# Performance work log

Measured on AMD Instinct MI355X. Metric: run time of the kernel, lower is better.

The kernel has to match this reference:

```python
import jax, jax.numpy as jnp
import numpy as np

GROUPS = 32
EPS = 1e-5
N_HEADS = 8


def setup_inputs() -> dict:
    key = jax.random.key(0)
    ks = jax.random.split(key, 12)
    B, H, W, C = 16, 64, 64, 512
    Nctx, Dctx = 77, 768
    s_c = 1.0 / np.sqrt(C)
    s_ctx = 1.0 / np.sqrt(Dctx)
    return {
        "x": jax.random.normal(ks[0], (B, H, W, C), jnp.float32),
        "context": jax.random.normal(ks[1], (B, Nctx, Dctx), jnp.float32),
        "gn_scale": jnp.ones((C,), jnp.float32),
        "gn_bias": jnp.zeros((C,), jnp.float32),
        "wq": jax.random.normal(ks[2], (C, C), jnp.float32) * s_c,
        "bq": jnp.zeros((C,), jnp.float32),
        "wk": jax.random.normal(ks[3], (Dctx, C), jnp.float32) * s_ctx,
        "bk": jnp.zeros((C,), jnp.float32),
        "wv": jax.random.normal(ks[4], (Dctx, C), jnp.float32) * s_ctx,
        "bv": jnp.zeros((C,), jnp.float32),
        "wo": jax.random.normal(ks[5], (C, C), jnp.float32) * s_c,
        "bo": jnp.zeros((C,), jnp.float32),
    }


def _group_norm(x, scale, bias):
    B, H, W, C = x.shape
    xg = x.reshape(B, H, W, GROUPS, C // GROUPS)
    mean = jnp.mean(xg, axis=(1, 2, 4), keepdims=True)
    var = jnp.var(xg, axis=(1, 2, 4), keepdims=True)
    xn = (xg - mean) * jax.lax.rsqrt(var + EPS)
    return xn.reshape(B, H, W, C) * scale + bias


def reference(x, context, gn_scale, gn_bias, wq, bq, wk, bk, wv, bv, wo, bo):
    B, H, W, C = x.shape
    head_dim = C // N_HEADS
    h = _group_norm(x, gn_scale, gn_bias)
    h_flat = h.reshape(B, H * W, C)
    Q = h_flat @ wq + bq                      # [B, N, C]
    K = context @ wk + bk                     # [B, Nctx, C]
    V = context @ wv + bv

    def split_heads(t):
        b, n, c = t.shape
        return t.reshape(b, n, N_HEADS, head_dim).transpose(0, 2, 1, 3)

    Qh, Kh, Vh = split_heads(Q), split_heads(K), split_heads(V)
    scale = 1.0 / jnp.sqrt(jnp.asarray(head_dim, x.dtype))
    scores = jnp.einsum('bhid,bhjd->bhij', Qh, Kh) * scale
    attn = jax.nn.softmax(scores, axis=-1)
    out = jnp.einsum('bhij,bhjd->bhid', attn, Vh)  # [B, h, N, d]
    out = out.transpose(0, 2, 1, 3).reshape(B, H * W, C)
    out = out @ wo + bo
    return out.reshape(B, H, W, C) + x
```

## Files before the change

kernel.cpp:

```cpp
#include <hip/hip_runtime.h>
#include <hip/hip_bf16.h>

typedef __attribute__((ext_vector_type(4))) float f32x4;
typedef __attribute__((ext_vector_type(8))) short bf16x8;
typedef unsigned short u16;

#define AS1 __attribute__((address_space(1)))
#define AS3 __attribute__((address_space(3)))

#define B_    16
#define HW_   4096
#define C_    512
#define NCTX  77
#define DCTX  768
#define NH    8
#define HD    64
#define EPSV  1e-5f

__device__ inline u16 f2bf(float f) {
    union { float f; unsigned u; } v; v.f = f;
    unsigned r = v.u + 0x7fffu + ((v.u >> 16) & 1u);
    return (u16)(r >> 16);
}
__device__ inline float bf2f(u16 h) {
    union { unsigned u; float f; } v; v.u = ((unsigned)h) << 16;
    return v.f;
}

__global__ __launch_bounds__(256) void gn_stats(const float* __restrict__ x,
                                                float* __restrict__ mean,
                                                float* __restrict__ rstd) {
    int b = blockIdx.x >> 5, g = blockIdx.x & 31;
    const float* px = x + (size_t)b * HW_ * C_ + g * 16;
    float s = 0.f, ss = 0.f;
    for (int t = threadIdx.x; t < HW_ * 4; t += 256) {
        int hw = t >> 2, c4 = (t & 3) * 4;
        const float4 v = *(const float4*)(px + (size_t)hw * C_ + c4);
        s  += v.x + v.y + v.z + v.w;
        ss += v.x * v.x + v.y * v.y + v.z * v.z + v.w * v.w;
    }
    for (int off = 32; off; off >>= 1) { s += __shfl_xor(s, off); ss += __shfl_xor(ss, off); }
    __shared__ float red[2][4];
    int wv = threadIdx.x >> 6, lane = threadIdx.x & 63;
    if (lane == 0) { red[0][wv] = s; red[1][wv] = ss; }
    __syncthreads();
    if (threadIdx.x == 0) {
        float S = red[0][0] + red[0][1] + red[0][2] + red[0][3];
        float SS = red[1][0] + red[1][1] + red[1][2] + red[1][3];
        float mn = S / 65536.f;
        float var = SS / 65536.f - mn * mn;
        mean[blockIdx.x] = mn;
        rstd[blockIdx.x] = rsqrtf(var + EPSV);
    }
}

__global__ __launch_bounds__(256) void transpose_all(const float* __restrict__ wq,
                                                     const float* __restrict__ wk,
                                                     const float* __restrict__ wv,
                                                     const float* __restrict__ wo,
                                                     u16* __restrict__ wqT,
                                                     u16* __restrict__ wkT,
                                                     u16* __restrict__ wvT,
                                                     u16* __restrict__ woT) {
    int idx = blockIdx.x * 256 + threadIdx.x;
    if (idx < 262144) {
        int k = idx >> 9, n = idx & 511;
        wqT[(size_t)n * 512 + k] = f2bf(wq[idx]);
    } else if (idx < 655360) {
        int i = idx - 262144;
        int k = i >> 9, n = i & 511;
        wkT[(size_t)n * 768 + k] = f2bf(wk[i]);
    } else if (idx < 1048576) {
        int i = idx - 655360;
        int k = i >> 9, n = i & 511;
        wvT[(size_t)n * 768 + k] = f2bf(wv[i]);
    } else if (idx < 1310720) {
        int i = idx - 1048576;
        int k = i >> 9, n = i & 511;
        woT[(size_t)n * 512 + k] = f2bf(wo[i]);
    }
}

__global__ __launch_bounds__(256) void gemm_kv(const float* __restrict__ A,
                                               const u16* __restrict__ wkT,
                                               const u16* __restrict__ wvT,
                                               const float* __restrict__ bk,
                                               const float* __restrict__ bv,
                                               u16* __restrict__ kb,
                                               u16* __restrict__ vb) {
    constexpr int M = 1232, K = 768;
    __shared__ __align__(16) u16 As[128][40];
    __shared__ __align__(16) u16 Bs[128][40];
    int bx = blockIdx.x;
    const u16* Bt = (bx < 4) ? wkT : wvT;
    const float* bias = (bx < 4) ? bk : bv;
    u16* out = (bx < 4) ? kb : vb;
    int tid = threadIdx.x, lane = tid & 63, wid = tid >> 6;
    int wm = wid >> 1, wn = wid & 1;
    int row0 = blockIdx.y * 128, col0 = (bx & 3) * 128;
    int q = lane >> 4, r16 = lane & 15;

    f32x4 acc[4][4];
#pragma unroll
    for (int i = 0; i < 4; i++)
#pragma unroll
        for (int j = 0; j < 4; j++) acc[i][j] = (f32x4){0.f, 0.f, 0.f, 0.f};

    for (int k0 = 0; k0 < K; k0 += 32) {
#pragma unroll
        for (int it = 0; it < 2; ++it) {
            int e = it * 256 + tid;
            int rr = e >> 2, kc = (e & 3) * 8;
            int ga = row0 + rr; if (ga > M - 1) ga = M - 1;
            float4 a0 = *(const float4*)(A + (size_t)ga * K + k0 + kc);
            float4 a1 = *(const float4*)(A + (size_t)ga * K + k0 + kc + 4);
            bf16x8 av;
            av[0] = (short)f2bf(a0.x); av[1] = (short)f2bf(a0.y);
            av[2] = (short)f2bf(a0.z); av[3] = (short)f2bf(a0.w);
            av[4] = (short)f2bf(a1.x); av[5] = (short)f2bf(a1.y);
            av[6] = (short)f2bf(a1.z); av[7] = (short)f2bf(a1.w);
            *(bf16x8*)&As[rr][kc] = av;
            int gb = col0 + rr;
            bf16x8 bv8 = *(const bf16x8*)(Bt + (size_t)gb * K + k0 + kc);
            *(bf16x8*)&Bs[rr][kc] = bv8;
        }
        __syncthreads();
        bf16x8 afr[4], bfr[4];
#pragma unroll
        for (int mi = 0; mi < 4; mi++) afr[mi] = *(const bf16x8*)&As[wm * 64 + mi * 16 + r16][q * 8];
#pragma unroll
        for (int ni = 0; ni < 4; ni++) bfr[ni] = *(const bf16x8*)&Bs[wn * 64 + ni * 16 + r16][q * 8];
#pragma unroll
        for (int mi = 0; mi < 4; mi++)
#pragma unroll
            for (int ni = 0; ni < 4; ni++)
                acc[mi][ni] = __builtin_amdgcn_mfma_f32_16x16x32_bf16(afr[mi], bfr[ni], acc[mi][ni], 0, 0, 0);
        __syncthreads();
    }

#pragma unroll
    for (int mi = 0; mi < 4; mi++) {
#pragma unroll
        for (int rr = 0; rr < 4; rr++) {
            int grow = row0 + wm * 64 + mi * 16 + q * 4 + rr;
            if (grow >= M) continue;
#pragma unroll
            for (int ni = 0; ni < 4; ni++) {
                int gcol = col0 + wn * 64 + ni * 16 + r16;
                float v = acc[mi][ni][rr] + bias[gcol];
                out[(size_t)grow * 512 + gcol] = f2bf(v);
            }
        }
    }
}

__global__ __launch_bounds__(256, 2) void gemm_fusedq(const float* __restrict__ x,
                                                      const float* __restrict__ mean,
                                                      const float* __restrict__ rstd,
                                                      const float* __restrict__ gns,
                                                      const float* __restrict__ gnb,
                                                      const u16* __restrict__ Bt,
                                                      const float* __restrict__ bias,
                                                      u16* __restrict__ out) {
    constexpr int K = 512;
    __shared__ __align__(16) u16 LA[2][8192];
    __shared__ __align__(16) u16 LB[2][8192];
    int tid = threadIdx.x, lane = tid & 63, wid = tid >> 6;
    int wr = wid >> 1, wc = wid & 1;
    int q = lane >> 4, r16 = lane & 15;

    int orig = blockIdx.x;
    int wg = (orig & 7) * 256 + (orig >> 3);
    int bx = wg & 3, by = wg >> 2;
    int row0 = by * 128, col0 = bx * 128;

    int srow = tid >> 3;
    int schunk = (tid & 7) ^ (srow & 7);
    const u16* gB = Bt + (size_t)(col0 + srow) * K + schunk * 8;
    const int lo = tid * 8;

    int c8 = tid & 7;
    int rbase = (tid >> 3) * 4;
    const float* xb = x + (size_t)(row0 + rbase) * 512 + c8 * 8;
    int bg0 = (row0 >> 12) * 32;

    f32x4 acc[4][4];
#pragma unroll
    for (int i = 0; i < 4; i++)
#pragma unroll
        for (int j = 0; j < 4; j++) acc[i][j] = (f32x4){0.f, 0.f, 0.f, 0.f};

    float4 ar[8];
    float mn, rs;
    float4 s0v, s1v, b0v, b1v;

#define LOADA(kt) do { _Pragma("unroll")                                          \
    for (int i_ = 0; i_ < 4; ++i_) {                                              \
        ar[2 * i_]     = *(const float4*)(xb + (kt) * 64 + (size_t)i_ * 512);     \
        ar[2 * i_ + 1] = *(const float4*)(xb + (kt) * 64 + (size_t)i_ * 512 + 4); \
    } } while (0)

#define LOADP(kt) do { int c0_ = (kt) * 64 + c8 * 8; int bg_ = bg0 + (c0_ >> 4);  \
    mn = mean[bg_]; rs = rstd[bg_];                                               \
    s0v = *(const float4*)(gns + c0_); s1v = *(const float4*)(gns + c0_ + 4);     \
    b0v = *(const float4*)(gnb + c0_); b1v = *(const float4*)(gnb + c0_ + 4);     \
  } while (0)

#define WRITEA(nbuf) do {                                                         \
    float m2_[8], a2_[8];                                                         \
    m2_[0]=rs*s0v.x; m2_[1]=rs*s0v.y; m2_[2]=rs*s0v.z; m2_[3]=rs*s0v.w;           \
    m2_[4]=rs*s1v.x; m2_[5]=rs*s1v.y; m2_[6]=rs*s1v.z; m2_[7]=rs*s1v.w;           \
    a2_[0]=b0v.x-mn*m2_[0]; a2_[1]=b0v.y-mn*m2_[1];                               \
    a2_[2]=b0v.z-mn*m2_[2]; a2_[3]=b0v.w-mn*m2_[3];                               \
    a2_[4]=b1v.x-mn*m2_[4]; a2_[5]=b1v.y-mn*m2_[5];                               \
    a2_[6]=b1v.z-mn*m2_[6]; a2_[7]=b1v.w-mn*m2_[7];                               \
    _Pragma("unroll")                                                             \
    for (int i_ = 0; i_ < 4; ++i_) {                                              \
        int row_ = rbase + i_;                                                    \
        bf16x8 pk_;                                                               \
        pk_[0]=(short)f2bf(ar[2*i_].x  *m2_[0]+a2_[0]);                           \
        pk_[1]=(short)f2bf(ar[2*i_].y  *m2_[1]+a2_[1]);                           \
        pk_[2]=(short)f2bf(ar[2*i_].z  *m2_[2]+a2_[2]);                           \
        pk_[3]=(short)f2bf(ar[2*i_].w  *m2_[3]+a2_[3]);                           \
        pk_[4]=(short)f2bf(ar[2*i_+1].x*m2_[4]+a2_[4]);                           \
        pk_[5]=(short)f2bf(ar[2*i_+1].y*m2_[5]+a2_[5]);                           \
        pk_[6]=(short)f2bf(ar[2*i_+1].z*m2_[6]+a2_[6]);                           \
        pk_[7]=(short)f2bf(ar[2*i_+1].w*m2_[7]+a2_[7]);                           \
        *(bf16x8*)&LA[nbuf][row_ * 64 + ((c8 ^ (row_ & 7)) * 8)] = pk_;           \
    } } while (0)

#define STG_B(kt, s) __builtin_amdgcn_global_load_lds( \
        (const AS1 void*)(gB + (kt) * 64 + (size_t)((s) * 32) * K), \
        (AS3 void*)(&LB[(kt) & 1][(s) * 2048 + lo]), 16, 0, 0)

#define PHASE_(buf, h, ks) do {                                                            \
    bf16x8 afr[2], bfr[4];                                                                 \
    const int ch_ = (((ks) * 4 + q) ^ (r16 & 7)) * 8;                                      \
    _Pragma("unroll")                                                                      \
    for (int mi = 0; mi < 2; mi++)                                                         \
        afr[mi] = *(const bf16x8*)&LA[buf][(wr * 64 + ((h) * 2 + mi) * 16 + r16) * 64 + ch_]; \
    _Pragma("unroll")                                                                      \
    for (int ni = 0; ni < 4; ni++)                                                         \
        bfr[ni] = *(const bf16x8*)&LB[buf][(wc * 64 + ni * 16 + r16) * 64 + ch_];          \
    __builtin_amdgcn_s_setprio(1);                                                         \
    _Pragma("unroll")                                                                      \
    for (int mi = 0; mi < 2; mi++)                                                         \
      _Pragma("unroll")                                                                    \
      for (int ni = 0; ni < 4; ni++)                                                       \
        acc[(h) * 2 + mi][ni] =                                                            \
            __builtin_amdgcn_mfma_f32_16x16x32_bf16(afr[mi], bfr[ni], acc[(h) * 2 + mi][ni], 0, 0, 0); \
    __builtin_amdgcn_s_setprio(0);                                                         \
  } while (0)

    LOADA(0); LOADP(0);
    asm volatile("" ::: "memory");
    STG_B(0, 0); STG_B(0, 1); STG_B(0, 2); STG_B(0, 3);
    asm volatile("s_waitcnt vmcnt(4)" ::: "memory");
    WRITEA(0);
    asm volatile("s_waitcnt lgkmcnt(0)" ::: "memory");

#pragma unroll
    for (int t = 0; t < 7; ++t) {
        const int buf = t & 1;
        LOADA(t + 1); LOADP(t + 1);
        asm volatile("" ::: "memory");
        STG_B(t + 1, 0); STG_B(t + 1, 1); STG_B(t + 1, 2); STG_B(t + 1, 3);
        asm volatile("s_waitcnt vmcnt(18)" ::: "memory");
        __builtin_amdgcn_s_barrier();
        asm volatile("" ::: "memory");
        PHASE_(buf, 0, 0); PHASE_(buf, 1, 0); PHASE_(buf, 0, 1); PHASE_(buf, 1, 1);
        asm volatile("s_waitcnt vmcnt(4)" ::: "memory");
        WRITEA(buf ^ 1);
        asm volatile("s_waitcnt lgkmcnt(0)" ::: "memory");
        __builtin_amdgcn_s_barrier();
        asm volatile("" ::: "memory");
    }
    asm volatile("s_waitcnt vmcnt(0) lgkmcnt(0)" ::: "memory");
    __builtin_amdgcn_s_barrier();
    asm volatile("" ::: "memory");
    PHASE_(1, 0, 0); PHASE_(1, 1, 0); PHASE_(1, 0, 1); PHASE_(1, 1, 1);
#undef LOADA
#undef LOADP
#undef WRITEA
#undef STG_B
#undef PHASE_

#pragma unroll
    for (int mi = 0; mi < 4; mi++) {
#pragma unroll
        for (int rr = 0; rr < 4; rr++) {
            int grow = row0 + wr * 64 + mi * 16 + q * 4 + rr;
#pragma unroll
            for (int ni = 0; ni < 4; ni++) {
                int gcol = col0 + wc * 64 + ni * 16 + r16;
                float v = acc[mi][ni][rr] + bias[gcol];
                out[(size_t)grow * 512 + gcol] = f2bf(v);
            }
        }
    }
}

__global__ __launch_bounds__(256, 4) void gemm_ring(const u16* __restrict__ A,
                                                    const u16* __restrict__ Bt,
                                                    const float* __restrict__ bias,
                                                    const float* __restrict__ res,
                                                    float* __restrict__ out) {
    constexpr int K = 512;
    __shared__ __align__(16) u16 LA[2][4096];
    __shared__ __align__(16) u16 LB[2][4096];
    int tid = threadIdx.x, lane = tid & 63, wid = tid >> 6;
    int wr = wid >> 1, wc = wid & 1;
    int q = lane >> 4, r16 = lane & 15;

    int orig = blockIdx.x;
    int wg = (orig & 7) * 256 + (orig >> 3);
    int bx = wg & 3, by = wg >> 2;
    int row0 = by * 128, col0 = bx * 128;

    int srow = tid >> 2;
    int schunk = (tid & 3) ^ (srow & 3);
    const u16* gA = A + (size_t)(row0 + srow) * K + schunk * 8;
    const u16* gB = Bt + (size_t)(col0 + srow) * K + schunk * 8;
    const int lo = tid * 8;

    f32x4 acc[4][4];
#pragma unroll
    for (int i = 0; i < 4; i++)
#pragma unroll
        for (int j = 0; j < 4; j++) acc[i][j] = (f32x4){0.f, 0.f, 0.f, 0.f};

#define STG(kt) do { int sl_ = (kt) & 1;                                              \
    __builtin_amdgcn_global_load_lds((const AS1 void*)(gA + (kt) * 32),               \
                                     (AS3 void*)(&LA[sl_][lo]), 16, 0, 0);            \
    __builtin_amdgcn_global_load_lds((const AS1 void*)(gA + (kt) * 32 + (size_t)64 * K), \
                                     (AS3 void*)(&LA[sl_][2048 + lo]), 16, 0, 0);     \
    __builtin_amdgcn_global_load_lds((const AS1 void*)(gB + (kt) * 32),               \
                                     (AS3 void*)(&LB[sl_][lo]), 16, 0, 0);            \
    __builtin_amdgcn_global_load_lds((const AS1 void*)(gB + (kt) * 32 + (size_t)64 * K), \
                                     (AS3 void*)(&LB[sl_][2048 + lo]), 16, 0, 0);     \
  } while (0)

#define COMPUTE(sl) do {                                                              \
    bf16x8 afr[4], bfr[4];                                                            \
    const int ch_ = (q ^ (r16 & 3)) * 8;                                              \
    _Pragma("unroll")                                                                 \
    for (int mi = 0; mi < 4; mi++)                                                    \
        afr[mi] = *(const bf16x8*)&LA[sl][(wr * 64 + mi * 16 + r16) * 32 + ch_];      \
    _Pragma("unroll")                                                                 \
    for (int ni = 0; ni < 4; ni++)                                                    \
        bfr[ni] = *(const bf16x8*)&LB[sl][(wc * 64 + ni * 16 + r16) * 32 + ch_];      \
    __builtin_amdgcn_s_setprio(1);                                                    \
    _Pragma("unroll")                                                                 \
    for (int mi = 0; mi < 4; mi++)                                                    \
      _Pragma("unroll")                                                               \
      for (int ni = 0; ni < 4; ni++)                                                  \
        acc[mi][ni] = __builtin_amdgcn_mfma_f32_16x16x32_bf16(afr[mi], bfr[ni], acc[mi][ni], 0, 0, 0); \
    __builtin_amdgcn_s_setprio(0);                                                    \
  } while (0)

    STG(0);
#pragma unroll
    for (int t = 0; t < 15; ++t) {
        STG(t + 1);
        asm volatile("s_waitcnt vmcnt(4)" ::: "memory");
        asm volatile("s_barrier" ::: "memory");
        COMPUTE(t & 1);
        asm volatile("s_barrier" ::: "memory");
    }
    asm volatile("s_waitcnt vmcnt(0)" ::: "memory");
    asm volatile("s_barrier" ::: "memory");
    COMPUTE(1);
#undef STG
#undef COMPUTE

#pragma unroll
    for (int mi = 0; mi < 4; mi++) {
#pragma unroll
        for (int rr = 0; rr < 4; rr++) {
            int grow = row0 + wr * 64 + mi * 16 + q * 4 + rr;
#pragma unroll
            for (int ni = 0; ni < 4; ni++) {
                int gcol = col0 + wc * 64 + ni * 16 + r16;
                float v = acc[mi][ni][rr] + bias[gcol];
                size_t idx = (size_t)grow * 512 + gcol;
                out[idx] = v + res[idx];
            }
        }
    }
}

__global__ __launch_bounds__(256) void attn_mfma(const u16* __restrict__ Qb,
                                                 const u16* __restrict__ Kb,
                                                 const u16* __restrict__ Vb,
                                                 u16* __restrict__ Ob) {
    __shared__ __align__(16) u16 Ks[80][72];
    __shared__ __align__(16) u16 VT[64][104];
    __shared__ __align__(16) u16 Ps[64][104];
    int tid = threadIdx.x, lane = tid & 63, wv = tid >> 6;
    int q = lane >> 4, r16 = lane & 15;
    int tile0 = blockIdx.x * 8;
    int bh = blockIdx.y;
    int b = bh >> 3, h = bh & 7;

    {
        unsigned* p0 = (unsigned*)&Ks[0][0];
        for (int i = tid; i < 2880; i += 256) p0[i] = 0u;
        unsigned* p1 = (unsigned*)&VT[0][0];
        for (int i = tid; i < 3328; i += 256) p1[i] = 0u;
        unsigned* p2 = (unsigned*)&Ps[0][0];
        for (int i = tid; i < 3328; i += 256) p2[i] = 0u;
    }
    __syncthreads();

    size_t kvbase = ((size_t)b * NCTX) * C_ + h * HD;
    for (int c = tid; c < NCTX * 8; c += 256) {
        int j = c >> 3, d8 = (c & 7) * 8;
        *(bf16x8*)&Ks[j][d8] = *(const bf16x8*)(Kb + kvbase + (size_t)j * C_ + d8);
    }
    for (int t = tid; t < NCTX * 64; t += 256) {
        int j = t >> 6, d = t & 63;
        VT[d][j] = Vb[kvbase + (size_t)j * C_ + d];
    }
    __syncthreads();

    const size_t tstep = (size_t)64 * C_;
    const u16* qp = Qb + ((size_t)b * HW_ + wv * 16 + r16) * C_ + h * HD + q * 8;
    bool v4 = (r16 < NCTX - 64);

    bf16x8 qc0 = *(const bf16x8*)(qp + (size_t)tile0 * tstep);
    bf16x8 qc1 = *(const bf16x8*)(qp + (size_t)tile0 * tstep + 32);

    for (int it = 0; it < 8; ++it) {
        int tile = tile0 + it;
        bf16x8 qn0 = qc0, qn1 = qc1;
        if (it < 7) {
            qn0 = *(const bf16x8*)(qp + (size_t)(tile + 1) * tstep);
            qn1 = *(const bf16x8*)(qp + (size_t)(tile + 1) * tstep + 32);
        }

        f32x4 accs[5];
#pragma unroll
        for (int nt = 0; nt < 5; ++nt) accs[nt] = (f32x4){0.f, 0.f, 0.f, 0.f};
#pragma unroll
        for (int nt = 0; nt < 5; ++nt) {
            bf16x8 kf = *(const bf16x8*)&Ks[nt * 16 + r16][q * 8];
            accs[nt] = __builtin_amdgcn_mfma_f32_16x16x32_bf16(qc0, kf, accs[nt], 0, 0, 0);
        }
#pragma unroll
        for (int nt = 0; nt < 5; ++nt) {
            bf16x8 kf = *(const bf16x8*)&Ks[nt * 16 + r16][32 + q * 8];
            accs[nt] = __builtin_amdgcn_mfma_f32_16x16x32_bf16(qc1, kf, accs[nt], 0, 0, 0);
        }

#pragma unroll
        for (int r = 0; r < 4; ++r) {
            float s[5];
#pragma unroll
            for (int nt = 0; nt < 5; ++nt) s[nt] = accs[nt][r] * 0.125f;
            float m = fmaxf(fmaxf(fmaxf(s[0], s[1]), fmaxf(s[2], s[3])), v4 ? s[4] : -3.0e38f);
#pragma unroll
            for (int off = 1; off < 16; off <<= 1) m = fmaxf(m, __shfl_xor(m, off));
            float e[5], sum = 0.f;
#pragma unroll
            for (int nt = 0; nt < 5; ++nt) {
                e[nt] = (nt < 4 || v4) ? __expf(s[nt] - m) : 0.f;
                sum += e[nt];
            }
#pragma unroll
            for (int off = 1; off < 16; off <<= 1) sum += __shfl_xor(sum, off);
            float inv = 1.0f / sum;
            int prow = wv * 16 + q * 4 + r;
#pragma unroll
            for (int nt = 0; nt < 5; ++nt)
                Ps[prow][nt * 16 + r16] = f2bf(e[nt] * inv);
        }

        f32x4 acco[4];
#pragma unroll
        for (int nt = 0; nt < 4; ++nt) acco[nt] = (f32x4){0.f, 0.f, 0.f, 0.f};
#pragma unroll
        for (int ks = 0; ks < 3; ++ks) {
            bf16x8 pf = *(const bf16x8*)&Ps[wv * 16 + r16][ks * 32 + q * 8];
#pragma unroll
            for (int nt = 0; nt < 4; ++nt) {
                bf16x8 vf = *(const bf16x8*)&VT[nt * 16 + r16][ks * 32 + q * 8];
                acco[nt] = __builtin_amdgcn_mfma_f32_16x16x32_bf16(pf, vf, acco[nt], 0, 0, 0);
            }
        }

        int row0 = tile * 64 + wv * 16;
#pragma unroll
        for (int nt = 0; nt < 4; ++nt)
#pragma unroll
            for (int r = 0; r < 4; ++r) {
                int row = row0 + q * 4 + r;
                int col = h * HD + nt * 16 + r16;
                Ob[((size_t)b * HW_ + row) * C_ + col] = f2bf(acco[nt][r]);
            }
        qc0 = qn0; qc1 = qn1;
    }
}

extern "C" void kernel_launch(void* const* d_in, const int* in_sizes, int n_in,
                              void* d_out, int out_size, void* d_ws, size_t ws_size,
                              hipStream_t stream) {
    const float* x   = (const float*)d_in[0];
    const float* ctx = (const float*)d_in[1];
    const float* gns = (const float*)d_in[2];
    const float* gnb = (const float*)d_in[3];
    const float* wq  = (const float*)d_in[4];
    const float* bq  = (const float*)d_in[5];
    const float* wk  = (const float*)d_in[6];
    const float* bk  = (const float*)d_in[7];
    const float* wv  = (const float*)d_in[8];
    const float* bv  = (const float*)d_in[9];
    const float* wo  = (const float*)d_in[10];
    const float* bo  = (const float*)d_in[11];

    char* ws = (char*)d_ws;
    float* mean = (float*)(ws + 0);
    float* rstd = (float*)(ws + 2048);
    u16* wqT  = (u16*)(ws + 4096);
    u16* wkT  = (u16*)(ws + 528384);
    u16* wvT  = (u16*)(ws + 1314816);
    u16* woT  = (u16*)(ws + 2101248);
    u16* aob  = (u16*)(ws + 4517888);
    u16* qb   = (u16*)(ws + 71626752);
    u16* kb   = (u16*)(ws + 138735616);
    u16* vb   = (u16*)(ws + 139997184);

    gn_stats<<<512, 256, 0, stream>>>(x, mean, rstd);
    transpose_all<<<5120, 256, 0, stream>>>(wq, wk, wv, wo, wqT, wkT, wvT, woT);

    gemm_fusedq<<<2048, 256, 0, stream>>>(x, mean, rstd, gns, gnb, wqT, bq, qb);
    gemm_kv<<<dim3(8, 10), 256, 0, stream>>>(ctx, wkT, wvT, bk, bv, kb, vb);

    attn_mfma<<<dim3(8, 128), 256, 0, stream>>>(qb, kb, vb, aob);

    gemm_ring<<<2048, 256, 0, stream>>>(aob, woT, bo, x, (float*)d_out);
}
```

Before: 291.3 us.

## Fuse Q projection with attention and merge stats/transpose kernels

```diff
diff --git a/kernel.cpp b/kernel.cpp
--- a/kernel.cpp
+++ b/kernel.cpp
@@ -22,62 +22,59 @@
     unsigned r = v.u + 0x7fffu + ((v.u >> 16) & 1u);
     return (u16)(r >> 16);
 }
-__device__ inline float bf2f(u16 h) {
-    union { unsigned u; float f; } v; v.u = ((unsigned)h) << 16;
-    return v.f;
-}
-
-__global__ __launch_bounds__(256) void gn_stats(const float* __restrict__ x,
+
+__global__ __launch_bounds__(256) void gn_trans(const float* __restrict__ x,
                                                 float* __restrict__ mean,
-                                                float* __restrict__ rstd) {
-    int b = blockIdx.x >> 5, g = blockIdx.x & 31;
-    const float* px = x + (size_t)b * HW_ * C_ + g * 16;
-    float s = 0.f, ss = 0.f;
-    for (int t = threadIdx.x; t < HW_ * 4; t += 256) {
-        int hw = t >> 2, c4 = (t & 3) * 4;
-        const float4 v = *(const float4*)(px + (size_t)hw * C_ + c4);
-        s  += v.x + v.y + v.z + v.w;
-        ss += v.x * v.x + v.y * v.y + v.z * v.z + v.w * v.w;
-    }
-    for (int off = 32; off; off >>= 1) { s += __shfl_xor(s, off); ss += __shfl_xor(ss, off); }
-    __shared__ float red[2][4];
-    int wv = threadIdx.x >> 6, lane = threadIdx.x & 63;
-    if (lane == 0) { red[0][wv] = s; red[1][wv] = ss; }
-    __syncthreads();
-    if (threadIdx.x == 0) {
-        float S = red[0][0] + red[0][1] + red[0][2] + red[0][3];
-        float SS = red[1][0] + red[1][1] + red[1][2] + red[1][3];
-        float mn = S / 65536.f;
-        float var = SS / 65536.f - mn * mn;
-        mean[blockIdx.x] = mn;
-        rstd[blockIdx.x] = rsqrtf(var + EPSV);
-    }
-}
-
-__global__ __launch_bounds__(256) void transpose_all(const float* __restrict__ wq,
-                                                     const float* __restrict__ wk,
-                                                     const float* __restrict__ wv,
-                                                     const float* __restrict__ wo,
-                                                     u16* __restrict__ wqT,
-                                                     u16* __restrict__ wkT,
-                                                     u16* __restrict__ wvT,
-                                                     u16* __restrict__ woT) {
-    int idx = blockIdx.x * 256 + threadIdx.x;
-    if (idx < 262144) {
-        int k = idx >> 9, n = idx & 511;
-        wqT[(size_t)n * 512 + k] = f2bf(wq[idx]);
-    } else if (idx < 655360) {
-        int i = idx - 262144;
-        int k = i >> 9, n = i & 511;
-        wkT[(size_t)n * 768 + k] = f2bf(wk[i]);
-    } else if (idx < 1048576) {
-        int i = idx - 655360;
-        int k = i >> 9, n = i & 511;
-        wvT[(size_t)n * 768 + k] = f2bf(wv[i]);
-    } else if (idx < 1310720) {
-        int i = idx - 1048576;
-        int k = i >> 9, n = i & 511;
-        woT[(size_t)n * 512 + k] = f2bf(wo[i]);
+                                                float* __restrict__ rstd,
+                                                const float* __restrict__ wq,
+                                                const float* __restrict__ wk,
+                                                const float* __restrict__ wv,
+                                                const float* __restrict__ wo,
+                                                u16* __restrict__ wqT,
+                                                u16* __restrict__ wkT,
+                                                u16* __restrict__ wvT,
+                                                u16* __restrict__ woT) {
+    if (blockIdx.x < 512) {
+        int b = blockIdx.x >> 5, g = blockIdx.x & 31;
+        const float* px = x + (size_t)b * HW_ * C_ + g * 16;
+        float s = 0.f, ss = 0.f;
+        for (int t = threadIdx.x; t < HW_ * 4; t += 256) {
+            int hw = t >> 2, c4 = (t & 3) * 4;
+            const float4 v = *(const float4*)(px + (size_t)hw * C_ + c4);
+            s  += v.x + v.y + v.z + v.w;
+            ss += v.x * v.x + v.y * v.y + v.z * v.z + v.w * v.w;
+        }
+        for (int off = 32; off; off >>= 1) { s += __shfl_xor(s, off); ss += __shfl_xor(ss, off); }
+        __shared__ float red[2][4];
+        int wv_ = threadIdx.x >> 6, lane = threadIdx.x & 63;
+        if (lane == 0) { red[0][wv_] = s; red[1][wv_] = ss; }
+        __syncthreads();
+        if (threadIdx.x == 0) {
+            float S = red[0][0] + red[0][1] + red[0][2] + red[0][3];
+            float SS = red[1][0] + red[1][1] + red[1][2] + red[1][3];
+            float mn = S / 65536.f;
+            float var = SS / 65536.f - mn * mn;
+            mean[blockIdx.x] = mn;
+            rstd[blockIdx.x] = rsqrtf(var + EPSV);
+        }
+    } else {
+        int idx = (blockIdx.x - 512) * 256 + threadIdx.x;
+        if (idx < 262144) {
+            int k = idx >> 9, n = idx & 511;
+            wqT[(size_t)n * 512 + k] = f2bf(wq[idx]);
+        } else if (idx < 655360) {
+            int i = idx - 262144;
+            int k = i >> 9, n = i & 511;
+            wkT[(size_t)n * 768 + k] = f2bf(wk[i]);
+        } else if (idx < 1048576) {
+            int i = idx - 655360;
+            int k = i >> 9, n = i & 511;
+            wvT[(size_t)n * 768 + k] = f2bf(wv[i]);
+        } else if (idx < 1310720) {
+            int i = idx - 1048576;
+            int k = i >> 9, n = i & 511;
+            woT[(size_t)n * 512 + k] = f2bf(wo[i]);
+        }
     }
 }
 
@@ -154,122 +151,145 @@
     }
 }
 
-__global__ __launch_bounds__(256, 2) void gemm_fusedq(const float* __restrict__ x,
+__global__ __launch_bounds__(256, 2) void fused_qattn(const float* __restrict__ x,
                                                       const float* __restrict__ mean,
                                                       const float* __restrict__ rstd,
                                                       const float* __restrict__ gns,
                                                       const float* __restrict__ gnb,
-                                                      const u16* __restrict__ Bt,
-                                                      const float* __restrict__ bias,
-                                                      u16* __restrict__ out) {
-    constexpr int K = 512;
-    __shared__ __align__(16) u16 LA[2][8192];
-    __shared__ __align__(16) u16 LB[2][8192];
+                                                      const u16* __restrict__ wqT,
+                                                      const float* __restrict__ bq,
+                                                      const u16* __restrict__ kb,
+                                                      const u16* __restrict__ vb,
+                                                      u16* __restrict__ aob) {
+    __shared__ __align__(16) u16 Ks[80][72];
+    __shared__ __align__(16) u16 VT[64][96];
+    __shared__ __align__(16) u16 Qs[128][72];
+    __shared__ __align__(16) u16 Ps[64][96];
+    __shared__ __align__(16) u16 LA[2][4096];
+    __shared__ __align__(16) u16 LB[2][2048];
     int tid = threadIdx.x, lane = tid & 63, wid = tid >> 6;
     int wr = wid >> 1, wc = wid & 1;
     int q = lane >> 4, r16 = lane & 15;
 
     int orig = blockIdx.x;
-    int wg = (orig & 7) * 256 + (orig >> 3);
-    int bx = wg & 3, by = wg >> 2;
-    int row0 = by * 128, col0 = bx * 128;
-
-    int srow = tid >> 3;
-    int schunk = (tid & 7) ^ (srow & 7);
-    const u16* gB = Bt + (size_t)(col0 + srow) * K + schunk * 8;
-    const int lo = tid * 8;
-
-    int c8 = tid & 7;
-    int rbase = (tid >> 3) * 4;
-    const float* xb = x + (size_t)(row0 + rbase) * 512 + c8 * 8;
-    int bg0 = (row0 >> 12) * 32;
-
-    f32x4 acc[4][4];
+    int wg = (orig & 7) * 512 + (orig >> 3);
+    int by = wg >> 3, h = wg & 7;
+    int row0 = by * 128;
+    int b = by >> 5;
+
+    {
+        unsigned* p0 = (unsigned*)&Ks[0][0];
+        for (int i = tid; i < 2880; i += 256) p0[i] = 0u;
+        unsigned* p1 = (unsigned*)&VT[0][0];
+        for (int i = tid; i < 3072; i += 256) p1[i] = 0u;
+        unsigned* p2 = (unsigned*)&Ps[0][0];
+        for (int i = tid; i < 3072; i += 256) p2[i] = 0u;
+    }
+    __syncthreads();
+
+    size_t kvbase = (size_t)b * NCTX * C_ + h * HD;
+    for (int c = tid; c < NCTX * 8; c += 256) {
+        int j = c >> 3, d8 = (c & 7) * 8;
+        *(bf16x8*)&Ks[j][d8] = *(const bf16x8*)(kb + kvbase + (size_t)j * C_ + d8);
+    }
+    for (int t = tid; t < NCTX * 64; t += 256) {
+        int j = t >> 6, d = t & 63;
+        VT[d][j] = vb[kvbase + (size_t)j * C_ + d];
+    }
+    asm volatile("s_waitcnt vmcnt(0) lgkmcnt(0)" ::: "memory");
+    __syncthreads();
+
+    int c8 = tid & 3;
+    int r0l = (tid >> 2) * 2;
+    const float* xb = x + (size_t)(row0 + r0l) * 512 + c8 * 8;
+    int bg0 = b * 32;
+    int srB = tid >> 2;
+    int cB = (tid & 3) ^ (srB & 3);
+    const u16* gB = wqT + (size_t)(h * 64 + srB) * 512 + cB * 8;
+
+    f32x4 acc[4][2];
 #pragma unroll
     for (int i = 0; i < 4; i++)
 #pragma unroll
-        for (int j = 0; j < 4; j++) acc[i][j] = (f32x4){0.f, 0.f, 0.f, 0.f};
-
-    float4 ar[8];
+        for (int j = 0; j < 2; j++) acc[i][j] = (f32x4){0.f, 0.f, 0.f, 0.f};
+
+    float4 ar0, ar1, ar2, ar3;
     float mn, rs;
     float4 s0v, s1v, b0v, b1v;
 
-#define LOADA(kt) do { _Pragma("unroll")                                          \
-    for (int i_ = 0; i_ < 4; ++i_) {                                              \
-        ar[2 * i_]     = *(const float4*)(xb + (kt) * 64 + (size_t)i_ * 512);     \
-        ar[2 * i_ + 1] = *(const float4*)(xb + (kt) * 64 + (size_t)i_ * 512 + 4); \
-    } } while (0)
-
-#define LOADP(kt) do { int c0_ = (kt) * 64 + c8 * 8; int bg_ = bg0 + (c0_ >> 4);  \
-    mn = mean[bg_]; rs = rstd[bg_];                                               \
-    s0v = *(const float4*)(gns + c0_); s1v = *(const float4*)(gns + c0_ + 4);     \
-    b0v = *(const float4*)(gnb + c0_); b1v = *(const float4*)(gnb + c0_ + 4);     \
+#define LOADA(kt) do {                                      \
+    ar0 = *(const float4*)(xb + (kt) * 32);                 \
+    ar1 = *(const float4*)(xb + (kt) * 32 + 4);             \
+    ar2 = *(const float4*)(xb + (kt) * 32 + 512);           \
+    ar3 = *(const float4*)(xb + (kt) * 32 + 516);           \
   } while (0)
 
-#define WRITEA(nbuf) do {                                                         \
-    float m2_[8], a2_[8];                                                         \
-    m2_[0]=rs*s0v.x; m2_[1]=rs*s0v.y; m2_[2]=rs*s0v.z; m2_[3]=rs*s0v.w;           \
-    m2_[4]=rs*s1v.x; m2_[5]=rs*s1v.y; m2_[6]=rs*s1v.z; m2_[7]=rs*s1v.w;           \
-    a2_[0]=b0v.x-mn*m2_[0]; a2_[1]=b0v.y-mn*m2_[1];                               \
-    a2_[2]=b0v.z-mn*m2_[2]; a2_[3]=b0v.w-mn*m2_[3];                               \
-    a2_[4]=b1v.x-mn*m2_[4]; a2_[5]=b1v.y-mn*m2_[5];                               \
-    a2_[6]=b1v.z-mn*m2_[6]; a2_[7]=b1v.w-mn*m2_[7];                               \
-    _Pragma("unroll")                                                             \
-    for (int i_ = 0; i_ < 4; ++i_) {                                              \
-        int row_ = rbase + i_;                                                    \
-        bf16x8 pk_;                                                               \
-        pk_[0]=(short)f2bf(ar[2*i_].x  *m2_[0]+a2_[0]);                           \
-        pk_[1]=(short)f2bf(ar[2*i_].y  *m2_[1]+a2_[1]);                           \
-        pk_[2]=(short)f2bf(ar[2*i_].z  *m2_[2]+a2_[2]);                           \
-        pk_[3]=(short)f2bf(ar[2*i_].w  *m2_[3]+a2_[3]);                           \
-        pk_[4]=(short)f2bf(ar[2*i_+1].x*m2_[4]+a2_[4]);                           \
-        pk_[5]=(short)f2bf(ar[2*i_+1].y*m2_[5]+a2_[5]);                           \
-        pk_[6]=(short)f2bf(ar[2*i_+1].z*m2_[6]+a2_[6]);                           \
-        pk_[7]=(short)f2bf(ar[2*i_+1].w*m2_[7]+a2_[7]);                           \
-        *(bf16x8*)&LA[nbuf][row_ * 64 + ((c8 ^ (row_ & 7)) * 8)] = pk_;           \
-    } } while (0)
-
-#define STG_B(kt, s) __builtin_amdgcn_global_load_lds( \
-        (const AS1 void*)(gB + (kt) * 64 + (size_t)((s) * 32) * K), \
-        (AS3 void*)(&LB[(kt) & 1][(s) * 2048 + lo]), 16, 0, 0)
-
-#define PHASE_(buf, h, ks) do {                                                            \
-    bf16x8 afr[2], bfr[4];                                                                 \
-    const int ch_ = (((ks) * 4 + q) ^ (r16 & 7)) * 8;                                      \
+#define LOADP(kt) do { int c0_ = (kt) * 32 + c8 * 8; int bg_ = bg0 + (c0_ >> 4); \
+    mn = mean[bg_]; rs = rstd[bg_];                                              \
+    s0v = *(const float4*)(gns + c0_); s1v = *(const float4*)(gns + c0_ + 4);    \
+    b0v = *(const float4*)(gnb + c0_); b1v = *(const float4*)(gnb + c0_ + 4);    \
+  } while (0)
+
+#define WRITEA(nbuf) do {                                                        \
+    float m_[8], a_[8];                                                          \
+    m_[0]=rs*s0v.x; m_[1]=rs*s0v.y; m_[2]=rs*s0v.z; m_[3]=rs*s0v.w;              \
+    m_[4]=rs*s1v.x; m_[5]=rs*s1v.y; m_[6]=rs*s1v.z; m_[7]=rs*s1v.w;              \
+    a_[0]=b0v.x-mn*m_[0]; a_[1]=b0v.y-mn*m_[1];                                  \
+    a_[2]=b0v.z-mn*m_[2]; a_[3]=b0v.w-mn*m_[3];                                  \
+    a_[4]=b1v.x-mn*m_[4]; a_[5]=b1v.y-mn*m_[5];                                  \
+    a_[6]=b1v.z-mn*m_[6]; a_[7]=b1v.w-mn*m_[7];                                  \
+    bf16x8 p0_, p1_;                                                             \
+    p0_[0]=(short)f2bf(ar0.x*m_[0]+a_[0]); p0_[1]=(short)f2bf(ar0.y*m_[1]+a_[1]);\
+    p0_[2]=(short)f2bf(ar0.z*m_[2]+a_[2]); p0_[3]=(short)f2bf(ar0.w*m_[3]+a_[3]);\
+    p0_[4]=(short)f2bf(ar1.x*m_[4]+a_[4]); p0_[5]=(short)f2bf(ar1.y*m_[5]+a_[5]);\
+    p0_[6]=(short)f2bf(ar1.z*m_[6]+a_[6]); p0_[7]=(short)f2bf(ar1.w*m_[7]+a_[7]);\
+    p1_[0]=(short)f2bf(ar2.x*m_[0]+a_[0]); p1_[1]=(short)f2bf(ar2.y*m_[1]+a_[1]);\
+    p1_[2]=(short)f2bf(ar2.z*m_[2]+a_[2]); p1_[3]=(short)f2bf(ar2.w*m_[3]+a_[3]);\
+    p1_[4]=(short)f2bf(ar3.x*m_[4]+a_[4]); p1_[5]=(short)f2bf(ar3.y*m_[5]+a_[5]);\
+    p1_[6]=(short)f2bf(ar3.z*m_[6]+a_[6]); p1_[7]=(short)f2bf(ar3.w*m_[7]+a_[7]);\
+    *(bf16x8*)&LA[nbuf][r0l * 32 + ((c8 ^ (r0l & 3)) * 8)] = p0_;                \
+    *(bf16x8*)&LA[nbuf][(r0l + 1) * 32 + ((c8 ^ ((r0l + 1) & 3)) * 8)] = p1_;    \
+  } while (0)
+
+#define STG_B(kt) __builtin_amdgcn_global_load_lds( \
+        (const AS1 void*)(gB + (kt) * 32), (AS3 void*)(&LB[(kt) & 1][tid * 8]), 16, 0, 0)
+
+#define COMPUTE(buf) do {                                                                  \
+    bf16x8 afr[4], bfr[2];                                                                 \
+    const int ch_ = (q ^ (r16 & 3)) * 8;                                                   \
     _Pragma("unroll")                                                                      \
-    for (int mi = 0; mi < 2; mi++)                                                         \
-        afr[mi] = *(const bf16x8*)&LA[buf][(wr * 64 + ((h) * 2 + mi) * 16 + r16) * 64 + ch_]; \
+    for (int mi = 0; mi < 4; mi++)                                                         \
+        afr[mi] = *(const bf16x8*)&LA[buf][(wr * 64 + mi * 16 + r16) * 32 + ch_];          \
     _Pragma("unroll")                                                                      \
-    for (int ni = 0; ni < 4; ni++)                                                         \
-        bfr[ni] = *(const bf16x8*)&LB[buf][(wc * 64 + ni * 16 + r16) * 64 + ch_];          \
+    for (int ni = 0; ni < 2; ni++)                                                         \
+        bfr[ni] = *(const bf16x8*)&LB[buf][(wc * 32 + ni * 16 + r16) * 32 + ch_];          \
     __builtin_amdgcn_s_setprio(1);                                                         \
     _Pragma("unroll")                                                                      \
-    for (int mi = 0; mi < 2; mi++)                                                         \
+    for (int mi = 0; mi < 4; mi++)                                                         \
       _Pragma("unroll")                                                                    \
-      for (int ni = 0; ni < 4; ni++)                                                       \
-        acc[(h) * 2 + mi][ni] =                                                            \
-            __builtin_amdgcn_mfma_f32_16x16x32_bf16(afr[mi], bfr[ni], acc[(h) * 2 + mi][ni], 0, 0, 0); \
+      for (int ni = 0; ni < 2; ni++)                                                       \
+        acc[mi][ni] = __builtin_amdgcn_mfma_f32_16x16x32_bf16(afr[mi], bfr[ni], acc[mi][ni], 0, 0, 0); \
     __builtin_amdgcn_s_setprio(0);                                                         \
   } while (0)
 
     LOADA(0); LOADP(0);
     asm volatile("" ::: "memory");
-    STG_B(0, 0); STG_B(0, 1); STG_B(0, 2); STG_B(0, 3);
-    asm volatile("s_waitcnt vmcnt(4)" ::: "memory");
+    STG_B(0);
+    asm volatile("s_waitcnt vmcnt(1)" ::: "memory");
     WRITEA(0);
     asm volatile("s_waitcnt lgkmcnt(0)" ::: "memory");
 
 #pragma unroll
-    for (int t = 0; t < 7; ++t) {
+    for (int t = 0; t < 15; ++t) {
         const int buf = t & 1;
         LOADA(t + 1); LOADP(t + 1);
         asm volatile("" ::: "memory");
-        STG_B(t + 1, 0); STG_B(t + 1, 1); STG_B(t + 1, 2); STG_B(t + 1, 3);
-        asm volatile("s_waitcnt vmcnt(18)" ::: "memory");
+        STG_B(t + 1);
+        asm volatile("s_waitcnt vmcnt(11)" ::: "memory");
         __builtin_amdgcn_s_barrier();
         asm volatile("" ::: "memory");
-        PHASE_(buf, 0, 0); PHASE_(buf, 1, 0); PHASE_(buf, 0, 1); PHASE_(buf, 1, 1);
-        asm volatile("s_waitcnt vmcnt(4)" ::: "memory");
+        COMPUTE(buf);
+        asm volatile("s_waitcnt vmcnt(1)" ::: "memory");
         WRITEA(buf ^ 1);
         asm volatile("s_waitcnt lgkmcnt(0)" ::: "memory");
         __builtin_amdgcn_s_barrier();
@@ -278,25 +298,90 @@
     asm volatile("s_waitcnt vmcnt(0) lgkmcnt(0)" ::: "memory");
     __builtin_amdgcn_s_barrier();
     asm volatile("" ::: "memory");
-    PHASE_(1, 0, 0); PHASE_(1, 1, 0); PHASE_(1, 0, 1); PHASE_(1, 1, 1);
+    COMPUTE(1);
 #undef LOADA
 #undef LOADP
 #undef WRITEA
 #undef STG_B
-#undef PHASE_
-
-#pragma unroll
-    for (int mi = 0; mi < 4; mi++) {
-#pragma unroll
-        for (int rr = 0; rr < 4; rr++) {
-            int grow = row0 + wr * 64 + mi * 16 + q * 4 + rr;
-#pragma unroll
-            for (int ni = 0; ni < 4; ni++) {
-                int gcol = col0 + wc * 64 + ni * 16 + r16;
-                float v = acc[mi][ni][rr] + bias[gcol];
-                out[(size_t)grow * 512 + gcol] = f2bf(v);
+#undef COMPUTE
+
+#pragma unroll
+    for (int mi = 0; mi < 4; mi++)
+#pragma unroll
+        for (int ni = 0; ni < 2; ni++)
+#pragma unroll
+            for (int rr = 0; rr < 4; rr++) {
+                int row = wr * 64 + mi * 16 + q * 4 + rr;
+                int col = wc * 32 + ni * 16 + r16;
+                Qs[row][col] = f2bf(acc[mi][ni][rr] + bq[h * 64 + col]);
             }
-        }
+    __syncthreads();
+
+    bool v4 = (r16 < NCTX - 64);
+#pragma unroll
+    for (int rh = 0; rh < 2; ++rh) {
+        int rl0 = rh * 64 + wid * 16;
+        bf16x8 qf0 = *(const bf16x8*)&Qs[rl0 + r16][q * 8];
+        bf16x8 qf1 = *(const bf16x8*)&Qs[rl0 + r16][32 + q * 8];
+
+        f32x4 accs[5];
+#pragma unroll
+        for (int nt = 0; nt < 5; ++nt) accs[nt] = (f32x4){0.f, 0.f, 0.f, 0.f};
+#pragma unroll
+        for (int nt = 0; nt < 5; ++nt) {
+            bf16x8 kf = *(const bf16x8*)&Ks[nt * 16 + r16][q * 8];
+            accs[nt] = __builtin_amdgcn_mfma_f32_16x16x32_bf16(qf0, kf, accs[nt], 0, 0, 0);
+        }
+#pragma unroll
+        for (int nt = 0; nt < 5; ++nt) {
+            bf16x8 kf = *(const bf16x8*)&Ks[nt * 16 + r16][32 + q * 8];
+            accs[nt] = __builtin_amdgcn_mfma_f32_16x16x32_bf16(qf1, kf, accs[nt], 0, 0, 0);
+        }
+
+#pragma unroll
+        for (int r = 0; r < 4; ++r) {
+            float s[5];
+#pragma unroll
+            for (int nt = 0; nt < 5; ++nt) s[nt] = accs[nt][r] * 0.125f;
+            float m = fmaxf(fmaxf(fmaxf(s[0], s[1]), fmaxf(s[2], s[3])), v4 ? s[4] : -3.0e38f);
+#pragma unroll
+            for (int off = 1; off < 16; off <<= 1) m = fmaxf(m, __shfl_xor(m, off));
+            float e[5], sum = 0.f;
+#pragma unroll
+            for (int nt = 0; nt < 5; ++nt) {
+                e[nt] = (nt < 4 || v4) ? __expf(s[nt] - m) : 0.f;
+                sum += e[nt];
+            }
+#pragma unroll
+            for (int off = 1; off < 16; off <<= 1) sum += __shfl_xor(sum, off);
+            float inv = 1.0f / sum;
+            int prow = wid * 16 + q * 4 + r;
+#pragma unroll
+            for (int nt = 0; nt < 5; ++nt)
+                Ps[prow][nt * 16 + r16] = f2bf(e[nt] * inv);
+        }
+
+        f32x4 acco[4];
+#pragma unroll
+        for (int nt = 0; nt < 4; ++nt) acco[nt] = (f32x4){0.f, 0.f, 0.f, 0.f};
+#pragma unroll
+        for (int ks = 0; ks < 3; ++ks) {
+            bf16x8 pf = *(const bf16x8*)&Ps[wid * 16 + r16][ks * 32 + q * 8];
+#pragma unroll
+            for (int nt = 0; nt < 4; ++nt) {
+                bf16x8 vf = *(const bf16x8*)&VT[nt * 16 + r16][ks * 32 + q * 8];
+                acco[nt] = __builtin_amdgcn_mfma_f32_16x16x32_bf16(pf, vf, acco[nt], 0, 0, 0);
+            }
+        }
+
+#pragma unroll
+        for (int nt = 0; nt < 4; ++nt)
+#pragma unroll
+            for (int r = 0; r < 4; ++r) {
+                int row = row0 + rl0 + q * 4 + r;
+                int col = h * 64 + nt * 16 + r16;
+                aob[(size_t)row * 512 + col] = f2bf(acco[nt][r]);
+            }
     }
 }
 
@@ -389,118 +474,6 @@
     }
 }
 
-__global__ __launch_bounds__(256) void attn_mfma(const u16* __restrict__ Qb,
-                                                 const u16* __restrict__ Kb,
-                                                 const u16* __restrict__ Vb,
-                                                 u16* __restrict__ Ob) {
-    __shared__ __align__(16) u16 Ks[80][72];
-    __shared__ __align__(16) u16 VT[64][104];
-    __shared__ __align__(16) u16 Ps[64][104];
-    int tid = threadIdx.x, lane = tid & 63, wv = tid >> 6;
-    int q = lane >> 4, r16 = lane & 15;
-    int tile0 = blockIdx.x * 8;
-    int bh = blockIdx.y;
-    int b = bh >> 3, h = bh & 7;
-
-    {
-        unsigned* p0 = (unsigned*)&Ks[0][0];
-        for (int i = tid; i < 2880; i += 256) p0[i] = 0u;
-        unsigned* p1 = (unsigned*)&VT[0][0];
-        for (int i = tid; i < 3328; i += 256) p1[i] = 0u;
-        unsigned* p2 = (unsigned*)&Ps[0][0];
-        for (int i = tid; i < 3328; i += 256) p2[i] = 0u;
-    }
-    __syncthreads();
-
-    size_t kvbase = ((size_t)b * NCTX) * C_ + h * HD;
-    for (int c = tid; c < NCTX * 8; c += 256) {
-        int j = c >> 3, d8 = (c & 7) * 8;
-        *(bf16x8*)&Ks[j][d8] = *(const bf16x8*)(Kb + kvbase + (size_t)j * C_ + d8);
-    }
-    for (int t = tid; t < NCTX * 64; t += 256) {
-        int j = t >> 6, d = t & 63;
-        VT[d][j] = Vb[kvbase + (size_t)j * C_ + d];
-    }
-    __syncthreads();
-
-    const size_t tstep = (size_t)64 * C_;
-    const u16* qp = Qb + ((size_t)b * HW_ + wv * 16 + r16) * C_ + h * HD + q * 8;
-    bool v4 = (r16 < NCTX - 64);
-
-    bf16x8 qc0 = *(const bf16x8*)(qp + (size_t)tile0 * tstep);
-    bf16x8 qc1 = *(const bf16x8*)(qp + (size_t)tile0 * tstep + 32);
-
-    for (int it = 0; it < 8; ++it) {
-        int tile = tile0 + it;
-        bf16x8 qn0 = qc0, qn1 = qc1;
-        if (it < 7) {
-            qn0 = *(const bf16x8*)(qp + (size_t)(tile + 1) * tstep);
-            qn1 = *(const bf16x8*)(qp + (size_t)(tile + 1) * tstep + 32);
-        }
-
-        f32x4 accs[5];
-#pragma unroll
-        for (int nt = 0; nt < 5; ++nt) accs[nt] = (f32x4){0.f, 0.f, 0.f, 0.f};
-#pragma unroll
-        for (int nt = 0; nt < 5; ++nt) {
-            bf16x8 kf = *(const bf16x8*)&Ks[nt * 16 + r16][q * 8];
-            accs[nt] = __builtin_amdgcn_mfma_f32_16x16x32_bf16(qc0, kf, accs[nt], 0, 0, 0);
-        }
-#pragma unroll
-        for (int nt = 0; nt < 5; ++nt) {
-            bf16x8 kf = *(const bf16x8*)&Ks[nt * 16 + r16][32 + q * 8];
-            accs[nt] = __builtin_amdgcn_mfma_f32_16x16x32_bf16(qc1, kf, accs[nt], 0, 0, 0);
-        }
-
-#pragma unroll
-        for (int r = 0; r < 4; ++r) {
-            float s[5];
-#pragma unroll
-            for (int nt = 0; nt < 5; ++nt) s[nt] = accs[nt][r] * 0.125f;
-            float m = fmaxf(fmaxf(fmaxf(s[0], s[1]), fmaxf(s[2], s[3])), v4 ? s[4] : -3.0e38f);
-#pragma unroll
-            for (int off = 1; off < 16; off <<= 1) m = fmaxf(m, __shfl_xor(m, off));
-            float e[5], sum = 0.f;
-#pragma unroll
-            for (int nt = 0; nt < 5; ++nt) {
-                e[nt] = (nt < 4 || v4) ? __expf(s[nt] - m) : 0.f;
-                sum += e[nt];
-            }
-#pragma unroll
-            for (int off = 1; off < 16; off <<= 1) sum += __shfl_xor(sum, off);
-            float inv = 1.0f / sum;
-            int prow = wv * 16 + q * 4 + r;
-#pragma unroll
-            for (int nt = 0; nt < 5; ++nt)
-                Ps[prow][nt * 16 + r16] = f2bf(e[nt] * inv);
-        }
-
-        f32x4 acco[4];
-#pragma unroll
-        for (int nt = 0; nt < 4; ++nt) acco[nt] = (f32x4){0.f, 0.f, 0.f, 0.f};
-#pragma unroll
-        for (int ks = 0; ks < 3; ++ks) {
-            bf16x8 pf = *(const bf16x8*)&Ps[wv * 16 + r16][ks * 32 + q * 8];
-#pragma unroll
-            for (int nt = 0; nt < 4; ++nt) {
-                bf16x8 vf = *(const bf16x8*)&VT[nt * 16 + r16][ks * 32 + q * 8];
-                acco[nt] = __builtin_amdgcn_mfma_f32_16x16x32_bf16(pf, vf, acco[nt], 0, 0, 0);
-            }
-        }
-
-        int row0 = tile * 64 + wv * 16;
-#pragma unroll
-        for (int nt = 0; nt < 4; ++nt)
-#pragma unroll
-            for (int r = 0; r < 4; ++r) {
-                int row = row0 + q * 4 + r;
-                int col = h * HD + nt * 16 + r16;
-                Ob[((size_t)b * HW_ + row) * C_ + col] = f2bf(acco[nt][r]);
-            }
-        qc0 = qn0; qc1 = qn1;
-    }
-}
-
 extern "C" void kernel_launch(void* const* d_in, const int* in_sizes, int n_in,
                               void* d_out, int out_size, void* d_ws, size_t ws_size,
                               hipStream_t stream) {
@@ -525,17 +498,13 @@
     u16* wvT  = (u16*)(ws + 1314816);
     u16* woT  = (u16*)(ws + 2101248);
     u16* aob  = (u16*)(ws + 4517888);
-    u16* qb   = (u16*)(ws + 71626752);
     u16* kb   = (u16*)(ws + 138735616);
     u16* vb   = (u16*)(ws + 139997184);
 
-    gn_stats<<<512, 256, 0, stream>>>(x, mean, rstd);
-    transpose_all<<<5120, 256, 0, stream>>>(wq, wk, wv, wo, wqT, wkT, wvT, woT);
-
-    gemm_fusedq<<<2048, 256, 0, stream>>>(x, mean, rstd, gns, gnb, wqT, bq, qb);
+    gn_trans<<<5632, 256, 0, stream>>>(x, mean, rstd, wq, wk, wv, wo, wqT, wkT, wvT, woT);
     gemm_kv<<<dim3(8, 10), 256, 0, stream>>>(ctx, wkT, wvT, bk, bv, kb, vb);
 
-    attn_mfma<<<dim3(8, 128), 256, 0, stream>>>(qb, kb, vb, aob);
+    fused_qattn<<<4096, 256, 0, stream>>>(x, mean, rstd, gns, gnb, wqT, bq, kb, vb, aob);
 
     gemm_ring<<<2048, 256, 0, stream>>>(aob, woT, bo, x, (float*)d_out);
 }
```

Result: slower. 353.1 us (+21.2%).
